# Kernel tuning notes

Hardware: AMD Instinct MI355X
Metric: run time of the kernel (lower is better)

## Reference

```python
import jax, jax.numpy as jnp
import numpy as np
import math

N_LEVELS = 16
F_PER_LEVEL = 2
LOG2_T = 19
T = 1 << LOG2_T
BASE_RES = 16
MAX_RES = 2048
PER_LEVEL_SCALE = (MAX_RES / BASE_RES) ** (1.0 / (N_LEVELS - 1))
BOUND = 0.5
PRIMES = (np.uint32(1), np.uint32(2654435761), np.uint32(805459861))


def _weight_norm(v, g):
    # w = g * v / ||v||_row (torch weight_norm over dim=1)
    return v * (g / jnp.linalg.norm(v, axis=1))[:, None]


def _softplus100(x):
    # torch Softplus(beta=100)
    return jax.nn.softplus(100.0 * x) * 0.01


def hashgrid_encode(x01, table):
    # x01: [N,3] in [0,1]; table: [L, T, F]
    feats = []
    for l in range(N_LEVELS):
        scale = BASE_RES * (PER_LEVEL_SCALE ** l) - 1.0  # tcnn grid scale
        res = int(math.ceil(scale)) + 1
        pos = x01 * scale + 0.5
        pos_floor = jnp.floor(pos)
        w = pos - pos_floor                      # [N,3] trilinear fracs
        c0 = pos_floor.astype(jnp.uint32)        # [N,3] base corner
        dense = (res ** 3) <= T                  # static per level
        acc = jnp.zeros((x01.shape[0], F_PER_LEVEL), dtype=table.dtype)
        for corner in range(8):
            off = [(corner >> d) & 1 for d in range(3)]
            cx = c0[:, 0] + np.uint32(off[0])
            cy = c0[:, 1] + np.uint32(off[1])
            cz = c0[:, 2] + np.uint32(off[2])
            if dense:
                idx = cx + cy * np.uint32(res) + cz * np.uint32(res * res)
            else:
                idx = (cx * PRIMES[0]) ^ (cy * PRIMES[1]) ^ (cz * PRIMES[2])
                idx = idx & np.uint32(T - 1)
            wc = ((w[:, 0] if off[0] else 1.0 - w[:, 0])
                  * (w[:, 1] if off[1] else 1.0 - w[:, 1])
                  * (w[:, 2] if off[2] else 1.0 - w[:, 2]))
            acc = acc + wc[:, None] * table[l, idx.astype(jnp.int32)]
        feats.append(acc)
    return jnp.concatenate(feats, axis=-1)  # [N, 32]


def setup_inputs() -> dict:
    key = jax.random.key(0)
    ks = jax.random.split(key, 4)
    N = 2 ** 21
    x = jax.random.uniform(ks[0], (N, 3), jnp.float32, -BOUND, BOUND)
    table = jax.random.uniform(ks[1], (N_LEVELS, T, F_PER_LEVEL), jnp.float32, -1e-4, 1e-4)
    d_in, d_hid, d_out = 35, 64, 13
    v1 = jax.random.normal(ks[2], (d_hid, d_in), jnp.float32) * (math.sqrt(2) / math.sqrt(d_hid))
    v2 = jax.random.normal(ks[3], (d_out, d_hid), jnp.float32) * 1e-4 + math.sqrt(math.pi) / math.sqrt(d_hid)
    g1 = jnp.linalg.norm(v1, axis=1)
    g2 = jnp.linalg.norm(v2, axis=1)
    b1 = jnp.zeros((d_hid,), jnp.float32)
    b2 = jnp.full((d_out,), -0.5, jnp.float32)  # -sphere_init_radius
    return {"x": x, "table": table, "v1": v1, "g1": g1, "b1": b1,
            "v2": v2, "g2": g2, "b2": b2}


def reference(x, table, v1, g1, b1, v2, g2, b2):
    x01 = jnp.clip((x + BOUND) / (2.0 * BOUND), 0.0, 1.0)
    enc = hashgrid_encode(x01, table)            # [N, 32]
    h = jnp.concatenate([x, enc], axis=1)        # [N, 35]
    w1 = _weight_norm(v1, g1)
    w2 = _weight_norm(v2, g2)
    h = _softplus100(h @ w1.T + b1)
    out = h @ w2.T + b2                          # [N, 13]
    return out
```

## Files before the change

### kernel.cpp

```cpp
#include <hip/hip_runtime.h>
#include <hip/hip_fp16.h>
#include <cstdint>
#include <cmath>

#define NLEV 16
#define NHASH 11
#define NHENC 9
#define NDENSE 5
#define TBL (1u << 19)
#define NBKT 32768
#define PTS 2

typedef _Float16 half8 __attribute__((ext_vector_type(8)));
typedef float f32x4 __attribute__((ext_vector_type(4)));

struct LevelParams {
    float scale[NLEV];
    uint32_t res[NLEV];
    uint32_t hashed_mask;
};

__device__ __forceinline__ int krow_map(int kr) {
    if (kr <= 2) return kr;
    if (kr >= 4 && kr <= 13) return kr - 1;
    if (kr >= 16 && kr <= 37) return kr - 3;
    return -1;
}

__global__ __launch_bounds__(256) void prep_weights(
    const float* __restrict__ v1, const float* __restrict__ g1,
    const float* __restrict__ v2, const float* __restrict__ g2,
    float* __restrict__ w1t, float* __restrict__ w2n,
    __half* __restrict__ w1f, __half* __restrict__ w2f)
{
    int t = threadIdx.x;
    if (t < 64) {
        float s = 0.f;
        #pragma unroll
        for (int k = 0; k < 35; ++k) { float v = v1[t*35 + k]; s += v*v; }
        float f = g1[t] / sqrtf(s);
        #pragma unroll
        for (int k = 0; k < 35; ++k) w1t[k*64 + t] = v1[t*35 + k] * f;
    } else if (t < 77) {
        int r = t - 64;
        float s = 0.f;
        #pragma unroll
        for (int k = 0; k < 64; ++k) { float v = v2[r*64 + k]; s += v*v; }
        float f = g2[r] / sqrtf(s);
        #pragma unroll
        for (int k = 0; k < 64; ++k) w2n[r*64 + k] = v2[r*64 + k] * f;
    }
    __syncthreads();
    for (int i = t; i < 4096; i += 256) {
        int j = i & 7, lane = (i >> 3) & 63, nt = (i >> 9) & 3, kc = i >> 11;
        int kr = kc*32 + ((lane >> 4) << 3) + j;
        int ncol = nt*16 + (lane & 15);
        int m = krow_map(kr);
        float val = (m >= 0) ? w1t[m*64 + ncol] : 0.f;
        w1f[i] = __float2half(val);
    }
    for (int i = t; i < 1024; i += 256) {
        int j = i & 7, lane = (i >> 3) & 63, kc = i >> 9;
        int kr = kc*32 + ((lane >> 4) << 3) + j;
        int col = lane & 15;
        float val = (col < 13) ? w2n[col*64 + kr] : 0.f;
        w2f[i] = __float2half(val);
    }
}

__device__ __forceinline__ uint32_t bucket_key(float u0, float u1, float u2)
{
    uint32_t a = min(31u, (uint32_t)(u0 * 32.f));
    uint32_t b = min(31u, (uint32_t)(u1 * 32.f));
    uint32_t c = min(31u, (uint32_t)(u2 * 32.f));
    return (a << 10) | (b << 5) | c;
}

__device__ __forceinline__ void load_u(const float* __restrict__ x, int pp,
                                       float& u0, float& u1, float& u2)
{
    float x0 = x[3*(size_t)pp + 0];
    float x1 = x[3*(size_t)pp + 1];
    float x2 = x[3*(size_t)pp + 2];
    u0 = fminf(fmaxf(x0 + 0.5f, 0.f), 1.f);
    u1 = fminf(fmaxf(x1 + 0.5f, 0.f), 1.f);
    u2 = fminf(fmaxf(x2 + 0.5f, 0.f), 1.f);
}

__global__ __launch_bounds__(256) void pack_and_hist(
    const float2* __restrict__ tin, uint32_t* __restrict__ tout, int n_entries,
    const float* __restrict__ x, uint32_t* __restrict__ hist, int N,
    int packBlocks)
{
    int b = blockIdx.x;
    if (b < packBlocks) {
        int i = b * 256 + threadIdx.x;
        if (i < n_entries) {
            float2 v = tin[i];
            __half2 h = __floats2half2_rn(v.x, v.y);
            tout[i] = *reinterpret_cast<uint32_t*>(&h);
        }
    } else {
        int i = (b - packBlocks) * 256 + threadIdx.x;
        if (i < N) {
            float u0, u1, u2;
            load_u(x, i, u0, u1, u2);
            atomicAdd(&hist[bucket_key(u0, u1, u2)], 1u);
        }
    }
}

__global__ __launch_bounds__(1024) void scan_hist(
    const uint32_t* __restrict__ hist, uint32_t* __restrict__ offs)
{
    __shared__ uint32_t part[1024];
    int t = threadIdx.x;
    uint32_t loc[32];
    uint32_t s = 0;
    #pragma unroll
    for (int k = 0; k < 32; ++k) { loc[k] = s; s += hist[t*32 + k]; }
    part[t] = s;
    __syncthreads();
    for (int d = 1; d < 1024; d <<= 1) {
        uint32_t v = (t >= d) ? part[t - d] : 0u;
        __syncthreads();
        part[t] += v;
        __syncthreads();
    }
    uint32_t base = (t > 0) ? part[t - 1] : 0u;
    #pragma unroll
    for (int k = 0; k < 32; ++k) offs[t*32 + k] = base + loc[k];
}

__global__ __launch_bounds__(256) void scatter_kernel(
    const float* __restrict__ x, uint32_t* __restrict__ offs,
    float4* __restrict__ xs4, int N)
{
    int i = blockIdx.x * 256 + threadIdx.x;
    if (i < N) {
        float x0 = x[3*(size_t)i + 0];
        float x1 = x[3*(size_t)i + 1];
        float x2 = x[3*(size_t)i + 2];
        float u0 = fminf(fmaxf(x0 + 0.5f, 0.f), 1.f);
        float u1 = fminf(fmaxf(x1 + 0.5f, 0.f), 1.f);
        float u2 = fminf(fmaxf(x2 + 0.5f, 0.f), 1.f);
        uint32_t pos = atomicAdd(&offs[bucket_key(u0, u1, u2)], 1u);
        xs4[pos] = make_float4(x0, x1, x2, __int_as_float(i));
    }
}

__device__ __forceinline__ void encode_one(
    float u0, float u1, float u2, float s, uint32_t res, bool hashed,
    const uint32_t* __restrict__ tl, float& a0, float& a1)
{
    float px = u0 * s + 0.5f;
    float py = u1 * s + 0.5f;
    float pz = u2 * s + 0.5f;
    float fx = floorf(px), fy = floorf(py), fz = floorf(pz);
    float wx1 = px - fx, wy1 = py - fy, wz1 = pz - fz;
    float wx0 = 1.f - wx1, wy0 = 1.f - wy1, wz0 = 1.f - wz1;
    uint32_t cx = (uint32_t)fx, cy = (uint32_t)fy, cz = (uint32_t)fz;

    uint32_t ix0, ix1, iy0, iy1, iz0, iz1;
    if (hashed) {
        ix0 = cx;                 ix1 = cx + 1u;
        iy0 = cy * 2654435761u;   iy1 = (cy + 1u) * 2654435761u;
        iz0 = cz * 805459861u;    iz1 = (cz + 1u) * 805459861u;
    } else {
        ix0 = cx;                 ix1 = cx + 1u;
        iy0 = cy * res;           iy1 = iy0 + res;
        uint32_t rr = res * res;
        iz0 = cz * rr;            iz1 = iz0 + rr;
    }

    uint32_t idxs[8];
    #pragma unroll
    for (int c = 0; c < 8; ++c) {
        uint32_t jx = (c & 1) ? ix1 : ix0;
        uint32_t jy = (c & 2) ? iy1 : iy0;
        uint32_t jz = (c & 4) ? iz1 : iz0;
        idxs[c] = hashed ? ((jx ^ jy ^ jz) & (TBL - 1u)) : (jx + jy + jz);
    }
    uint32_t raw[8];
    #pragma unroll
    for (int c = 0; c < 8; ++c) raw[c] = tl[idxs[c]];

    float wxy00 = wx0*wy0, wxy10 = wx1*wy0, wxy01 = wx0*wy1, wxy11 = wx1*wy1;
    a0 = 0.f; a1 = 0.f;
    #pragma unroll
    for (int c = 0; c < 8; ++c) {
        float wxy = (c & 2) ? ((c & 1) ? wxy11 : wxy01)
                            : ((c & 1) ? wxy10 : wxy00);
        float w = wxy * ((c & 4) ? wz1 : wz0);
        __half2 hv = *reinterpret_cast<__half2*>(&raw[c]);
        float2 v = __half22float2(hv);
        a0 += w * v.x;
        a1 += w * v.y;
    }
}

template <int SORTED>
__global__ __launch_bounds__(256) void encode_hashed(
    const float* __restrict__ x, const float4* __restrict__ xs4,
    const uint32_t* __restrict__ tpk,
    uint32_t* __restrict__ feats, int N, int chunks_per_level, LevelParams P)
{
    int bid = blockIdx.x;
    int li = bid / chunks_per_level;
    int l = li + 7;
    int base = (bid - li * chunks_per_level) * (256*PTS) + threadIdx.x;
    const uint32_t* tl = tpk + (size_t)l * TBL;
    float s = P.scale[l];

    int p[PTS];
    #pragma unroll
    for (int t = 0; t < PTS; ++t) p[t] = base + t * 256;

    uint2 Q[PTS][4];
    uint32_t par[PTS];
    float wx0[PTS], wx1[PTS], wyz[PTS][4];

    #pragma unroll
    for (int t = 0; t < PTS; ++t) {
        int pp = (p[t] < N) ? p[t] : (N - 1);
        float u0, u1, u2;
        if (SORTED) {
            float4 v4 = xs4[pp];
            u0 = fminf(fmaxf(v4.x + 0.5f, 0.f), 1.f);
            u1 = fminf(fmaxf(v4.y + 0.5f, 0.f), 1.f);
            u2 = fminf(fmaxf(v4.z + 0.5f, 0.f), 1.f);
        } else {
            load_u(x, pp, u0, u1, u2);
        }

        float px = u0 * s + 0.5f;
        float py = u1 * s + 0.5f;
        float pz = u2 * s + 0.5f;
        float fx = floorf(px), fy = floorf(py), fz = floorf(pz);
        float a1f = px - fx, b1f = py - fy, c1f = pz - fz;
        wx1[t] = a1f; wx0[t] = 1.f - a1f;
        float wy0 = 1.f - b1f, wz0 = 1.f - c1f;
        uint32_t cx = (uint32_t)fx, cy = (uint32_t)fy, cz = (uint32_t)fz;

        wyz[t][0] = wy0 * wz0;
        wyz[t][1] = b1f * wz0;
        wyz[t][2] = wy0 * c1f;
        wyz[t][3] = b1f * c1f;

        uint32_t hy0 = cy * 2654435761u, hy1 = (cy + 1u) * 2654435761u;
        uint32_t hz0 = cz * 805459861u,  hz1 = (cz + 1u) * 805459861u;
        uint32_t r[4] = { hy0 ^ hz0, hy1 ^ hz0, hy0 ^ hz1, hy1 ^ hz1 };

        par[t] = 0u;
        if (!(cx & 1u)) {
            #pragma unroll
            for (int k = 0; k < 4; ++k) {
                uint32_t v0 = (cx ^ r[k]) & (TBL - 1u);
                Q[t][k] = *reinterpret_cast<const uint2*>(tl + (v0 & ~1u));
                par[t] |= (v0 & 1u) << k;
            }
        } else {
            #pragma unroll
            for (int k = 0; k < 4; ++k) {
                uint32_t v0 = (cx ^ r[k]) & (TBL - 1u);
                uint32_t v1 = ((cx + 1u) ^ r[k]) & (TBL - 1u);
                Q[t][k].x = tl[v0];
                Q[t][k].y = tl[v1];
            }
        }
    }

    #pragma unroll
    for (int t = 0; t < PTS; ++t) {
        float a0 = 0.f, a1 = 0.f;
        #pragma unroll
        for (int k = 0; k < 4; ++k) {
            uint32_t swap = (par[t] >> k) & 1u;
            uint32_t b0 = swap ? Q[t][k].y : Q[t][k].x;
            uint32_t b1 = swap ? Q[t][k].x : Q[t][k].y;
            __half2 h0 = *reinterpret_cast<__half2*>(&b0);
            __half2 h1 = *reinterpret_cast<__half2*>(&b1);
            float2 c0 = __half22float2(h0);
            float2 c1 = __half22float2(h1);
            a0 += wyz[t][k] * (wx0[t] * c0.x + wx1[t] * c1.x);
            a1 += wyz[t][k] * (wx0[t] * c0.y + wx1[t] * c1.y);
        }
        __half2 hv = __floats2half2_rn(a0, a1);
        if (p[t] < N) {
            __builtin_nontemporal_store(*reinterpret_cast<uint32_t*>(&hv),
                                        &feats[(size_t)li * N + p[t]]);
        }
    }
}

__global__ __launch_bounds__(256) void mlp_mfma(
    const float4* __restrict__ xs4,
    const uint32_t* __restrict__ tpk,
    const uint32_t* __restrict__ feats,
    const __half* __restrict__ w1f,
    const __half* __restrict__ w2f,
    const float* __restrict__ b1,
    const float* __restrict__ b2,
    float* __restrict__ out, int N, LevelParams P)
{
    __shared__ uint4 ldsA[4][576];
    __shared__ int   ldsI[4][64];
    int wid = threadIdx.x >> 6, lane = threadIdx.x & 63;
    int wpt = blockIdx.x * 256 + wid * 64;
    int pt = wpt + lane;
    int pp = (pt < N) ? pt : (N - 1);

    float4 v4 = xs4[pp];
    float x0 = v4.x, x1 = v4.y, x2 = v4.z;
    ldsI[wid][lane] = __float_as_int(v4.w);
    float u0 = fminf(fmaxf(x0 + 0.5f, 0.f), 1.f);
    float u1 = fminf(fmaxf(x1 + 0.5f, 0.f), 1.f);
    float u2 = fminf(fmaxf(x2 + 0.5f, 0.f), 1.f);

    uint32_t dw[32];
    #pragma unroll
    for (int i = 0; i < 32; ++i) dw[i] = 0u;
    __half2 h01 = __floats2half2_rn(x0, x1);
    __half2 h2_ = __floats2half2_rn(x2, 0.f);
    dw[0] = *reinterpret_cast<uint32_t*>(&h01);
    dw[1] = *reinterpret_cast<uint32_t*>(&h2_);
    #pragma unroll
    for (int l = 0; l < NDENSE; ++l) {
        const uint32_t* tl = tpk + (size_t)l * TBL;
        float a0, a1;
        encode_one(u0, u1, u2, P.scale[l], P.res[l], false, tl, a0, a1);
        __half2 hv = __floats2half2_rn(a0, a1);
        dw[2 + l] = *reinterpret_cast<uint32_t*>(&hv);
    }
    #pragma unroll
    for (int l = 5; l <= 6; ++l) {
        const uint32_t* tl = tpk + (size_t)l * TBL;
        float a0, a1;
        encode_one(u0, u1, u2, P.scale[l], P.res[l], true, tl, a0, a1);
        __half2 hv = __floats2half2_rn(a0, a1);
        dw[8 + (l - 5)] = *reinterpret_cast<uint32_t*>(&hv);
    }
    #pragma unroll
    for (int li = 0; li < NHENC; ++li)
        dw[10 + li] = feats[(size_t)li * N + pp];

    #pragma unroll
    for (int c = 0; c < 8; ++c) {
        uint4 ch = make_uint4(dw[4*c], dw[4*c+1], dw[4*c+2], dw[4*c+3]);
        ldsA[wid][c*64 + lane] = ch;
    }

    const uint4* w1f4 = (const uint4*)w1f;
    half8 bf[4][2];
    #pragma unroll
    for (int nt = 0; nt < 4; ++nt)
        #pragma unroll
        for (int kc = 0; kc < 2; ++kc) {
            uint4 u = w1f4[(kc*4 + nt)*64 + lane];
            bf[nt][kc] = __builtin_bit_cast(half8, u);
        }

    f32x4 C[4][4];
    #pragma unroll
    for (int nt = 0; nt < 4; ++nt) {
        float bv = b1[nt*16 + (lane & 15)];
        #pragma unroll
        for (int m = 0; m < 4; ++m) C[m][nt] = f32x4{bv, bv, bv, bv};
    }

    #pragma unroll
    for (int m = 0; m < 4; ++m) {
        uint4 ua0 = ldsA[wid][((lane >> 4)      )*64 + m*16 + (lane & 15)];
        uint4 ua1 = ldsA[wid][((lane >> 4) + 4  )*64 + m*16 + (lane & 15)];
        half8 a0 = __builtin_bit_cast(half8, ua0);
        half8 a1 = __builtin_bit_cast(half8, ua1);
        #pragma unroll
        for (int nt = 0; nt < 4; ++nt) {
            C[m][nt] = __builtin_amdgcn_mfma_f32_16x16x32_f16(a0, bf[nt][0], C[m][nt], 0, 0, 0);
            C[m][nt] = __builtin_amdgcn_mfma_f32_16x16x32_f16(a1, bf[nt][1], C[m][nt], 0, 0, 0);
        }
    }

    #pragma unroll
    for (int m = 0; m < 4; ++m)
        #pragma unroll
        for (int nt = 0; nt < 4; ++nt)
            #pragma unroll
            for (int r = 0; r < 4; ++r) {
                float z = 100.f * C[m][nt][r];
                float t = __expf(-fabsf(z));
                C[m][nt][r] = (fmaxf(z, 0.f) + __logf(1.f + t)) * 0.01f;
            }

    uint32_t* hl = (uint32_t*)&ldsA[wid][0];
    bool evenl = (lane & 1) == 0;
    #pragma unroll
    for (int m = 0; m < 4; ++m)
        #pragma unroll
        for (int nt = 0; nt < 4; ++nt)
            #pragma unroll
            for (int r = 0; r < 4; ++r) {
                float self = C[m][nt][r];
                float other = __shfl_xor(self, 1);
                if (evenl) {
                    __half2 hp = __floats2half2_rn(self, other);
                    int prow = m*16 + ((lane >> 4) << 2) + r;
                    int colp = (nt*16 + (lane & 15)) >> 1;
                    hl[prow*36 + colp] = *reinterpret_cast<uint32_t*>(&hp);
                }
            }

    const uint4* w2f4 = (const uint4*)w2f;
    half8 b2f[2];
    #pragma unroll
    for (int kc = 0; kc < 2; ++kc) {
        uint4 u = w2f4[kc*64 + lane];
        b2f[kc] = __builtin_bit_cast(half8, u);
    }
    int col = lane & 15;
    float b2v = (col < 13) ? b2[col] : 0.f;

    #pragma unroll
    for (int m = 0; m < 4; ++m) {
        uint4 ua0 = ldsA[wid][(m*16 + col)*9 + 0 + (lane >> 4)];
        uint4 ua1 = ldsA[wid][(m*16 + col)*9 + 4 + (lane >> 4)];
        f32x4 c2 = f32x4{b2v, b2v, b2v, b2v};
        c2 = __builtin_amdgcn_mfma_f32_16x16x32_f16(
                 __builtin_bit_cast(half8, ua0), b2f[0], c2, 0, 0, 0);
        c2 = __builtin_amdgcn_mfma_f32_16x16x32_f16(
                 __builtin_bit_cast(half8, ua1), b2f[1], c2, 0, 0, 0);
        #pragma unroll
        for (int r = 0; r < 4; ++r) {
            int prow = m*16 + ((lane >> 4) << 2) + r;
            if (col < 13 && wpt + prow < N) {
                int og = ldsI[wid][prow];
                out[(size_t)og * 13 + col] = c2[r];
            }
        }
    }
}

__global__ __launch_bounds__(256) void mlp_dense_scalar(
    const float* __restrict__ x, const uint32_t* __restrict__ tpk,
    const uint32_t* __restrict__ feats,
    const float* __restrict__ w1t, const float* __restrict__ b1,
    const float* __restrict__ w2, const float* __restrict__ b2,
    float* __restrict__ out, int N, LevelParams P)
{
    int p = blockIdx.x * 256 + threadIdx.x;
    bool valid = (p < N);
    int pp = valid ? p : (N - 1);

    float u0, u1, u2;
    load_u(x, pp, u0, u1, u2);
    float x0 = x[3*(size_t)pp + 0];
    float x1 = x[3*(size_t)pp + 1];
    float x2 = x[3*(size_t)pp + 2];

    uint32_t rf[NHENC];
    #pragma unroll
    for (int li = 0; li < NHENC; ++li) rf[li] = feats[(size_t)li * N + pp];

    float h[64];
    #pragma unroll
    for (int j = 0; j < 64; ++j)
        h[j] = b1[j] + x0 * w1t[0*64 + j] + x1 * w1t[1*64 + j] + x2 * w1t[2*64 + j];

    #pragma unroll
    for (int l = 0; l < 7; ++l) {
        const uint32_t* tl = tpk + (size_t)l * TBL;
        float a0, a1;
        encode_one(u0, u1, u2, P.scale[l], P.res[l], l >= NDENSE, tl, a0, a1);
        const float* c0p = w1t + (3 + 2*l) * 64;
        const float* c1p = c0p + 64;
        #pragma unroll
        for (int j = 0; j < 64; ++j) h[j] += a0 * c0p[j] + a1 * c1p[j];
    }
    #pragma unroll
    for (int li = 0; li < NHENC; ++li) {
        __half2 hv = *reinterpret_cast<__half2*>(&rf[li]);
        float2 f = __half22float2(hv);
        int l = li + 7;
        const float* c0p = w1t + (3 + 2*l) * 64;
        const float* c1p = c0p + 64;
        #pragma unroll
        for (int j = 0; j < 64; ++j) h[j] += f.x * c0p[j] + f.y * c1p[j];
    }
    #pragma unroll
    for (int j = 0; j < 64; ++j) {
        float z = 100.f * h[j];
        float t = __expf(-fabsf(z));
        h[j] = (fmaxf(z, 0.f) + __logf(1.f + t)) * 0.01f;
    }
    float* op = out + (size_t)pp * 13;
    for (int o = 0; o < 13; ++o) {
        float a = b2[o];
        const float* wr = w2 + o * 64;
        #pragma unroll
        for (int k = 0; k < 64; ++k) a = fmaf(h[k], wr[k], a);
        if (valid) op[o] = a;
    }
}

template <int PACKED>
__global__ __launch_bounds__(256) void sdf_fused(
    const float* __restrict__ x, const void* __restrict__ table,
    const float* __restrict__ w1t, const float* __restrict__ b1,
    const float* __restrict__ w2, const float* __restrict__ b2,
    float* __restrict__ out, int N, LevelParams P)
{
    int i = blockIdx.x * 256 + threadIdx.x;
    bool valid = (i < N);
    int ii = valid ? i : (N - 1);

    float x0 = x[3*(size_t)ii + 0];
    float x1 = x[3*(size_t)ii + 1];
    float x2 = x[3*(size_t)ii + 2];
    float u0 = fminf(fmaxf(x0 + 0.5f, 0.f), 1.f);
    float u1 = fminf(fmaxf(x1 + 0.5f, 0.f), 1.f);
    float u2 = fminf(fmaxf(x2 + 0.5f, 0.f), 1.f);

    float h[64];
    #pragma unroll
    for (int j = 0; j < 64; ++j)
        h[j] = b1[j] + x0 * w1t[0*64 + j] + x1 * w1t[1*64 + j] + x2 * w1t[2*64 + j];

    for (int l = 0; l < NLEV; ++l) {
        bool hashed = (P.hashed_mask >> l) & 1u;
        float a0, a1;
        if (PACKED) {
            const uint32_t* tl = (const uint32_t*)table + (size_t)l * TBL;
            encode_one(u0, u1, u2, P.scale[l], P.res[l], hashed, tl, a0, a1);
        } else {
            const float* tl = (const float*)table + (size_t)l * (size_t)(TBL * 2u);
            float s = P.scale[l]; uint32_t res = P.res[l];
            float px = u0*s + 0.5f, py = u1*s + 0.5f, pz = u2*s + 0.5f;
            float fx = floorf(px), fy = floorf(py), fz = floorf(pz);
            float wx1 = px-fx, wy1 = py-fy, wz1 = pz-fz;
            float wx0 = 1.f-wx1, wy0 = 1.f-wy1, wz0 = 1.f-wz1;
            uint32_t cx = (uint32_t)fx, cy = (uint32_t)fy, cz = (uint32_t)fz;
            a0 = 0.f; a1 = 0.f;
            #pragma unroll
            for (int c = 0; c < 8; ++c) {
                uint32_t jx = cx + (c & 1);
                uint32_t jy = cy + ((c >> 1) & 1);
                uint32_t jz = cz + ((c >> 2) & 1);
                uint32_t idx = hashed
                    ? ((jx ^ (jy * 2654435761u) ^ (jz * 805459861u)) & (TBL - 1u))
                    : (jx + jy * res + jz * res * res);
                float w = ((c & 1) ? wx1 : wx0) * ((c & 2) ? wy1 : wy0)
                        * ((c & 4) ? wz1 : wz0);
                float2 v = *reinterpret_cast<const float2*>(tl + (size_t)idx * 2u);
                a0 += w * v.x; a1 += w * v.y;
            }
        }
        const float* c0p = w1t + (3 + 2*l) * 64;
        const float* c1p = c0p + 64;
        #pragma unroll
        for (int j = 0; j < 64; ++j) h[j] += a0 * c0p[j] + a1 * c1p[j];
    }

    #pragma unroll
    for (int j = 0; j < 64; ++j) {
        float z = 100.f * h[j];
        float t = __expf(-fabsf(z));
        h[j] = (fmaxf(z, 0.f) + __logf(1.f + t)) * 0.01f;
    }

    float* op = out + (size_t)ii * 13;
    for (int o = 0; o < 13; ++o) {
        float a = b2[o];
        const float* wr = w2 + o * 64;
        #pragma unroll
        for (int k = 0; k < 64; ++k) a += h[k] * wr[k];
        if (valid) op[o] = a;
    }
}

extern "C" void kernel_launch(void* const* d_in, const int* in_sizes, int n_in,
                              void* d_out, int out_size, void* d_ws, size_t ws_size,
                              hipStream_t stream)
{
    const float* x     = (const float*)d_in[0];
    const float* table = (const float*)d_in[1];
    const float* v1    = (const float*)d_in[2];
    const float* g1    = (const float*)d_in[3];
    const float* b1    = (const float*)d_in[4];
    const float* v2    = (const float*)d_in[5];
    const float* g2    = (const float*)d_in[6];
    const float* b2    = (const float*)d_in[7];
    float* out = (float*)d_out;
    int N = in_sizes[0] / 3;

    const int n_entries = NLEV * (int)TBL;
    const size_t packed_bytes = (size_t)n_entries * 4u;
    const size_t xs4_bytes    = (size_t)N * 16u;
    const size_t feats_bytes  = (size_t)NHENC * (size_t)N * 4u;
    const size_t hist_bytes   = (size_t)NBKT * 4u;
    const size_t w_bytes      = (35*64 + 13*64) * sizeof(float);
    const size_t wf_bytes     = (4096 + 1024) * sizeof(__half);

    size_t off_packed = 0;
    size_t off_xs4    = off_packed + packed_bytes;
    size_t off_feats  = off_xs4 + xs4_bytes;
    size_t off_w      = off_feats + feats_bytes;
    size_t off_wf     = off_w + w_bytes;
    size_t sorted_need = off_wf + wf_bytes;
    bool overlay_ok = feats_bytes >= 2 * hist_bytes;

    bool sorted_ok = (ws_size >= sorted_need) && overlay_ok;
    bool two_pass  = (ws_size >= packed_bytes + feats_bytes + w_bytes + wf_bytes);
    bool packed_ok = (ws_size >= packed_bytes + w_bytes + wf_bytes);

    uint32_t* tpk   = (uint32_t*)((char*)d_ws + off_packed);
    float4*   xs4   = (float4*)((char*)d_ws + off_xs4);
    uint32_t* feats;
    float* w1t;
    if (sorted_ok) {
        feats = (uint32_t*)((char*)d_ws + off_feats);
        w1t = (float*)((char*)d_ws + off_w);
    } else if (two_pass) {
        feats = (uint32_t*)((char*)d_ws + packed_bytes);
        w1t = (float*)((char*)d_ws + packed_bytes + feats_bytes);
    } else {
        feats = nullptr;
        w1t = (float*)((char*)d_ws + (packed_ok ? packed_bytes : 0));
    }
    uint32_t* hist = feats;
    uint32_t* offs = feats + NBKT;
    float* w2n = w1t + 35 * 64;
    __half* w1f = (__half*)(w2n + 13 * 64);
    __half* w2f = w1f + 4096;

    LevelParams P;
    P.hashed_mask = 0u;
    double pls = pow(128.0, 1.0 / 15.0);
    for (int l = 0; l < NLEV; ++l) {
        double sc = 16.0 * pow(pls, (double)l) - 1.0;
        P.scale[l] = (float)sc;
        uint32_t res = (uint32_t)(ceil(sc)) + 1u;
        P.res[l] = res;
        uint64_t r3 = (uint64_t)res * res * res;
        if (r3 > (uint64_t)TBL) P.hashed_mask |= (1u << l);
    }

    prep_weights<<<1, 256, 0, stream>>>(v1, g1, v2, g2, w1t, w2n, w1f, w2f);

    int chunks = (N + 255) / 256;
    int packBlocks = (n_entries + 255) / 256;
    if (sorted_ok) {
        hipMemsetAsync(hist, 0, hist_bytes, stream);
        pack_and_hist<<<packBlocks + chunks, 256, 0, stream>>>(
            (const float2*)table, tpk, n_entries, x, hist, N, packBlocks);
        scan_hist<<<1, 1024, 0, stream>>>(hist, offs);
        scatter_kernel<<<chunks, 256, 0, stream>>>(x, offs, xs4, N);
        int chunksE = (N + 256*PTS - 1) / (256*PTS);
        encode_hashed<1><<<chunksE * NHENC, 256, 0, stream>>>(
            x, xs4, tpk, feats, N, chunksE, P);
        mlp_mfma<<<chunks, 256, 0, stream>>>(
            xs4, tpk, feats, w1f, w2f, b1, b2, out, N, P);
    } else if (two_pass) {
        pack_and_hist<<<packBlocks, 256, 0, stream>>>(
            (const float2*)table, tpk, n_entries, x, nullptr, 0, packBlocks);
        int chunksE = (N + 256*PTS - 1) / (256*PTS);
        encode_hashed<0><<<chunksE * NHENC, 256, 0, stream>>>(
            x, nullptr, tpk, feats, N, chunksE, P);
        mlp_dense_scalar<<<chunks, 256, 0, stream>>>(
            x, tpk, feats, w1t, b1, w2n, b2, out, N, P);
    } else if (packed_ok) {
        pack_and_hist<<<packBlocks, 256, 0, stream>>>(
            (const float2*)table, tpk, n_entries, x, nullptr, 0, packBlocks);
        sdf_fused<1><<<chunks, 256, 0, stream>>>(
            x, (const void*)tpk, w1t, b1, w2n, b2, out, N, P);
    } else {
        sdf_fused<0><<<chunks, 256, 0, stream>>>(
            x, (const void*)table, w1t, b1, w2n, b2, out, N, P);
    }
}
```

Baseline: 709.9 us.

## Quantize hash table to int8 with global absmax scale

Replaces the fp16-packed hash table with an int8 packing of two features per entry. The per-tensor scale comes from a new max-abs reduction kernel over the fp32 table. This halves table footprint and gather bytes, and the paired-corner loads now cover four entries per 8-byte load. In exchange it adds a full extra pass over the table for the reduction and loses precision, since values are quantized to 8 bits with a single global scale.

```diff
diff --git a/kernel.cpp b/kernel.cpp
--- a/kernel.cpp
+++ b/kernel.cpp
@@ -4,7 +4,6 @@
 #include <cmath>
 
 #define NLEV 16
-#define NHASH 11
 #define NHENC 9
 #define NDENSE 5
 #define TBL (1u << 19)
@@ -68,6 +67,17 @@
     }
 }
 
+__global__ __launch_bounds__(256) void max_reduce(
+    const float* __restrict__ t, uint32_t* __restrict__ scaleU, int n)
+{
+    int i = blockIdx.x * 256 + threadIdx.x;
+    float m = 0.f;
+    for (int k = i; k < n; k += gridDim.x * 256) m = fmaxf(m, fabsf(t[k]));
+    #pragma unroll
+    for (int o = 32; o >= 1; o >>= 1) m = fmaxf(m, __shfl_xor(m, o));
+    if ((threadIdx.x & 63) == 0) atomicMax(scaleU, __float_as_uint(m));
+}
+
 __device__ __forceinline__ uint32_t bucket_key(float u0, float u1, float u2)
 {
     uint32_t a = min(31u, (uint32_t)(u0 * 32.f));
@@ -87,20 +97,31 @@
     u2 = fminf(fmaxf(x2 + 0.5f, 0.f), 1.f);
 }
 
+__device__ __forceinline__ uint32_t quant8(float v, float qs)
+{
+    int q = (int)rintf(v * qs);
+    q = max(-127, min(127, q));
+    return (uint32_t)(q & 0xff);
+}
+
 __global__ __launch_bounds__(256) void pack_and_hist(
-    const float2* __restrict__ tin, uint32_t* __restrict__ tout, int n_entries,
+    const float2* __restrict__ tin, uint32_t* __restrict__ tout, int n_half,
     const float* __restrict__ x, uint32_t* __restrict__ hist, int N,
-    int packBlocks)
+    int packBlocks, const uint32_t* __restrict__ scaleU)
 {
     int b = blockIdx.x;
     if (b < packBlocks) {
         int i = b * 256 + threadIdx.x;
-        if (i < n_entries) {
-            float2 v = tin[i];
-            __half2 h = __floats2half2_rn(v.x, v.y);
-            tout[i] = *reinterpret_cast<uint32_t*>(&h);
-        }
-    } else {
+        if (i < n_half) {
+            float smax = fmaxf(__uint_as_float(*scaleU), 1e-30f);
+            float qs = 127.f / smax;
+            float2 a = tin[2*(size_t)i];
+            float2 c = tin[2*(size_t)i + 1];
+            uint32_t w = quant8(a.x, qs) | (quant8(a.y, qs) << 8)
+                       | (quant8(c.x, qs) << 16) | (quant8(c.y, qs) << 24);
+            tout[i] = w;
+        }
+    } else if (hist) {
         int i = (b - packBlocks) * 256 + threadIdx.x;
         if (i < N) {
             float u0, u1, u2;
@@ -149,9 +170,9 @@
     }
 }
 
-__device__ __forceinline__ void encode_one(
+__device__ __forceinline__ void encode_one8(
     float u0, float u1, float u2, float s, uint32_t res, bool hashed,
-    const uint32_t* __restrict__ tl, float& a0, float& a1)
+    const uint16_t* __restrict__ t16, float deq, float& a0, float& a1)
 {
     float px = u0 * s + 0.5f;
     float py = u1 * s + 0.5f;
@@ -181,9 +202,9 @@
         uint32_t jz = (c & 4) ? iz1 : iz0;
         idxs[c] = hashed ? ((jx ^ jy ^ jz) & (TBL - 1u)) : (jx + jy + jz);
     }
-    uint32_t raw[8];
-    #pragma unroll
-    for (int c = 0; c < 8; ++c) raw[c] = tl[idxs[c]];
+    uint16_t raw[8];
+    #pragma unroll
+    for (int c = 0; c < 8; ++c) raw[c] = t16[idxs[c]];
 
     float wxy00 = wx0*wy0, wxy10 = wx1*wy0, wxy01 = wx0*wy1, wxy11 = wx1*wy1;
     a0 = 0.f; a1 = 0.f;
@@ -192,25 +213,29 @@
         float wxy = (c & 2) ? ((c & 1) ? wxy11 : wxy01)
                             : ((c & 1) ? wxy10 : wxy00);
         float w = wxy * ((c & 4) ? wz1 : wz0);
-        __half2 hv = *reinterpret_cast<__half2*>(&raw[c]);
-        float2 v = __half22float2(hv);
-        a0 += w * v.x;
-        a1 += w * v.y;
-    }
+        float f0 = (float)(int8_t)(raw[c] & 0xff);
+        float f1 = (float)(int8_t)(raw[c] >> 8);
+        a0 += w * f0;
+        a1 += w * f1;
+    }
+    a0 *= deq;
+    a1 *= deq;
 }
 
 template <int SORTED>
 __global__ __launch_bounds__(256) void encode_hashed(
     const float* __restrict__ x, const float4* __restrict__ xs4,
-    const uint32_t* __restrict__ tpk,
-    uint32_t* __restrict__ feats, int N, int chunks_per_level, LevelParams P)
+    const uint8_t* __restrict__ tpk8,
+    uint32_t* __restrict__ feats, int N, int chunks_per_level,
+    const uint32_t* __restrict__ scaleU, LevelParams P)
 {
     int bid = blockIdx.x;
     int li = bid / chunks_per_level;
     int l = li + 7;
     int base = (bid - li * chunks_per_level) * (256*PTS) + threadIdx.x;
-    const uint32_t* tl = tpk + (size_t)l * TBL;
+    const uint8_t* tb8 = tpk8 + (size_t)l * TBL * 2u;
     float s = P.scale[l];
+    float deq = __uint_as_float(*scaleU) * (1.f / 127.f);
 
     int p[PTS];
     #pragma unroll
@@ -251,23 +276,26 @@
         uint32_t hz0 = cz * 805459861u,  hz1 = (cz + 1u) * 805459861u;
         uint32_t r[4] = { hy0 ^ hz0, hy1 ^ hz0, hy0 ^ hz1, hy1 ^ hz1 };
 
-        par[t] = 0u;
-        if (!(cx & 1u)) {
+        uint32_t pr = 0u;
+        if ((cx & 3u) != 3u) {
             #pragma unroll
             for (int k = 0; k < 4; ++k) {
                 uint32_t v0 = (cx ^ r[k]) & (TBL - 1u);
-                Q[t][k] = *reinterpret_cast<const uint2*>(tl + (v0 & ~1u));
-                par[t] |= (v0 & 1u) << k;
+                uint32_t v1 = ((cx + 1u) ^ r[k]) & (TBL - 1u);
+                Q[t][k] = *reinterpret_cast<const uint2*>(tb8 + ((v0 & ~3u) << 1));
+                pr |= ((v0 & 3u) | ((v1 & 3u) << 2)) << (4*k);
             }
         } else {
             #pragma unroll
             for (int k = 0; k < 4; ++k) {
                 uint32_t v0 = (cx ^ r[k]) & (TBL - 1u);
                 uint32_t v1 = ((cx + 1u) ^ r[k]) & (TBL - 1u);
-                Q[t][k].x = tl[v0];
-                Q[t][k].y = tl[v1];
+                Q[t][k].x = *reinterpret_cast<const uint32_t*>(tb8 + ((v0 & ~1u) << 1));
+                Q[t][k].y = *reinterpret_cast<const uint32_t*>(tb8 + ((v1 & ~1u) << 1));
+                pr |= ((v0 & 1u) | (((v1 & 1u) | 2u) << 2)) << (4*k);
             }
         }
+        par[t] = pr;
     }
 
     #pragma unroll
@@ -275,17 +303,20 @@
         float a0 = 0.f, a1 = 0.f;
         #pragma unroll
         for (int k = 0; k < 4; ++k) {
-            uint32_t swap = (par[t] >> k) & 1u;
-            uint32_t b0 = swap ? Q[t][k].y : Q[t][k].x;
-            uint32_t b1 = swap ? Q[t][k].x : Q[t][k].y;
-            __half2 h0 = *reinterpret_cast<__half2*>(&b0);
-            __half2 h1 = *reinterpret_cast<__half2*>(&b1);
-            float2 c0 = __half22float2(h0);
-            float2 c1 = __half22float2(h1);
-            a0 += wyz[t][k] * (wx0[t] * c0.x + wx1[t] * c1.x);
-            a1 += wyz[t][k] * (wx0[t] * c0.y + wx1[t] * c1.y);
-        }
-        __half2 hv = __floats2half2_rn(a0, a1);
+            uint32_t pk = par[t] >> (4*k);
+            uint32_t j0 = pk & 3u, j1 = (pk >> 2) & 3u;
+            uint32_t w0 = (j0 & 2u) ? Q[t][k].y : Q[t][k].x;
+            uint32_t w1 = (j1 & 2u) ? Q[t][k].y : Q[t][k].x;
+            uint32_t e0 = (j0 & 1u) ? (w0 >> 16) : (w0 & 0xffffu);
+            uint32_t e1 = (j1 & 1u) ? (w1 >> 16) : (w1 & 0xffffu);
+            float c0x = (float)(int8_t)(e0 & 0xff);
+            float c0y = (float)(int8_t)(e0 >> 8);
+            float c1x = (float)(int8_t)(e1 & 0xff);
+            float c1y = (float)(int8_t)(e1 >> 8);
+            a0 += wyz[t][k] * (wx0[t] * c0x + wx1[t] * c1x);
+            a1 += wyz[t][k] * (wx0[t] * c0y + wx1[t] * c1y);
+        }
+        __half2 hv = __floats2half2_rn(a0 * deq, a1 * deq);
         if (p[t] < N) {
             __builtin_nontemporal_store(*reinterpret_cast<uint32_t*>(&hv),
                                         &feats[(size_t)li * N + p[t]]);
@@ -295,12 +326,13 @@
 
 __global__ __launch_bounds__(256) void mlp_mfma(
     const float4* __restrict__ xs4,
-    const uint32_t* __restrict__ tpk,
+    const uint8_t* __restrict__ tpk8,
     const uint32_t* __restrict__ feats,
     const __half* __restrict__ w1f,
     const __half* __restrict__ w2f,
     const float* __restrict__ b1,
     const float* __restrict__ b2,
+    const uint32_t* __restrict__ scaleU,
     float* __restrict__ out, int N, LevelParams P)
 {
     __shared__ uint4 ldsA[4][576];
@@ -316,6 +348,7 @@
     float u0 = fminf(fmaxf(x0 + 0.5f, 0.f), 1.f);
     float u1 = fminf(fmaxf(x1 + 0.5f, 0.f), 1.f);
     float u2 = fminf(fmaxf(x2 + 0.5f, 0.f), 1.f);
+    float deq = __uint_as_float(*scaleU) * (1.f / 127.f);
 
     uint32_t dw[32];
     #pragma unroll
@@ -326,17 +359,17 @@
     dw[1] = *reinterpret_cast<uint32_t*>(&h2_);
     #pragma unroll
     for (int l = 0; l < NDENSE; ++l) {
-        const uint32_t* tl = tpk + (size_t)l * TBL;
+        const uint16_t* t16 = (const uint16_t*)(tpk8 + (size_t)l * TBL * 2u);
         float a0, a1;
-        encode_one(u0, u1, u2, P.scale[l], P.res[l], false, tl, a0, a1);
+        encode_one8(u0, u1, u2, P.scale[l], P.res[l], false, t16, deq, a0, a1);
         __half2 hv = __floats2half2_rn(a0, a1);
         dw[2 + l] = *reinterpret_cast<uint32_t*>(&hv);
     }
     #pragma unroll
     for (int l = 5; l <= 6; ++l) {
-        const uint32_t* tl = tpk + (size_t)l * TBL;
+        const uint16_t* t16 = (const uint16_t*)(tpk8 + (size_t)l * TBL * 2u);
         float a0, a1;
-        encode_one(u0, u1, u2, P.scale[l], P.res[l], true, tl, a0, a1);
+        encode_one8(u0, u1, u2, P.scale[l], P.res[l], true, t16, deq, a0, a1);
         __half2 hv = __floats2half2_rn(a0, a1);
         dw[8 + (l - 5)] = *reinterpret_cast<uint32_t*>(&hv);
     }
@@ -441,10 +474,11 @@
 }
 
 __global__ __launch_bounds__(256) void mlp_dense_scalar(
-    const float* __restrict__ x, const uint32_t* __restrict__ tpk,
+    const float* __restrict__ x, const uint8_t* __restrict__ tpk8,
     const uint32_t* __restrict__ feats,
     const float* __restrict__ w1t, const float* __restrict__ b1,
     const float* __restrict__ w2, const float* __restrict__ b2,
+    const uint32_t* __restrict__ scaleU,
     float* __restrict__ out, int N, LevelParams P)
 {
     int p = blockIdx.x * 256 + threadIdx.x;
@@ -456,6 +490,7 @@
     float x0 = x[3*(size_t)pp + 0];
     float x1 = x[3*(size_t)pp + 1];
     float x2 = x[3*(size_t)pp + 2];
+    float deq = __uint_as_float(*scaleU) * (1.f / 127.f);
 
     uint32_t rf[NHENC];
     #pragma unroll
@@ -468,9 +503,9 @@
 
     #pragma unroll
     for (int l = 0; l < 7; ++l) {
-        const uint32_t* tl = tpk + (size_t)l * TBL;
+        const uint16_t* t16 = (const uint16_t*)(tpk8 + (size_t)l * TBL * 2u);
         float a0, a1;
-        encode_one(u0, u1, u2, P.scale[l], P.res[l], l >= NDENSE, tl, a0, a1);
+        encode_one8(u0, u1, u2, P.scale[l], P.res[l], l >= NDENSE, t16, deq, a0, a1);
         const float* c0p = w1t + (3 + 2*l) * 64;
         const float* c1p = c0p + 64;
         #pragma unroll
@@ -502,9 +537,8 @@
     }
 }
 
-template <int PACKED>
-__global__ __launch_bounds__(256) void sdf_fused(
-    const float* __restrict__ x, const void* __restrict__ table,
+__global__ __launch_bounds__(256) void sdf_fused_f32(
+    const float* __restrict__ x, const float* __restrict__ table,
     const float* __restrict__ w1t, const float* __restrict__ b1,
     const float* __restrict__ w2, const float* __restrict__ b2,
     float* __restrict__ out, int N, LevelParams P)
@@ -527,32 +561,26 @@
 
     for (int l = 0; l < NLEV; ++l) {
         bool hashed = (P.hashed_mask >> l) & 1u;
-        float a0, a1;
-        if (PACKED) {
-            const uint32_t* tl = (const uint32_t*)table + (size_t)l * TBL;
-            encode_one(u0, u1, u2, P.scale[l], P.res[l], hashed, tl, a0, a1);
-        } else {
-            const float* tl = (const float*)table + (size_t)l * (size_t)(TBL * 2u);
-            float s = P.scale[l]; uint32_t res = P.res[l];
-            float px = u0*s + 0.5f, py = u1*s + 0.5f, pz = u2*s + 0.5f;
-            float fx = floorf(px), fy = floorf(py), fz = floorf(pz);
-            float wx1 = px-fx, wy1 = py-fy, wz1 = pz-fz;
-            float wx0 = 1.f-wx1, wy0 = 1.f-wy1, wz0 = 1.f-wz1;
-            uint32_t cx = (uint32_t)fx, cy = (uint32_t)fy, cz = (uint32_t)fz;
-            a0 = 0.f; a1 = 0.f;
-            #pragma unroll
-            for (int c = 0; c < 8; ++c) {
-                uint32_t jx = cx + (c & 1);
-                uint32_t jy = cy + ((c >> 1) & 1);
-                uint32_t jz = cz + ((c >> 2) & 1);
-                uint32_t idx = hashed
-                    ? ((jx ^ (jy * 2654435761u) ^ (jz * 805459861u)) & (TBL - 1u))
-                    : (jx + jy * res + jz * res * res);
-                float w = ((c & 1) ? wx1 : wx0) * ((c & 2) ? wy1 : wy0)
-                        * ((c & 4) ? wz1 : wz0);
-                float2 v = *reinterpret_cast<const float2*>(tl + (size_t)idx * 2u);
-                a0 += w * v.x; a1 += w * v.y;
-            }
+        const float* tl = table + (size_t)l * (size_t)(TBL * 2u);
+        float s = P.scale[l]; uint32_t res = P.res[l];
+        float px = u0*s + 0.5f, py = u1*s + 0.5f, pz = u2*s + 0.5f;
+        float fx = floorf(px), fy = floorf(py), fz = floorf(pz);
+        float wx1 = px-fx, wy1 = py-fy, wz1 = pz-fz;
+        float wx0 = 1.f-wx1, wy0 = 1.f-wy1, wz0 = 1.f-wz1;
+        uint32_t cx = (uint32_t)fx, cy = (uint32_t)fy, cz = (uint32_t)fz;
+        float a0 = 0.f, a1 = 0.f;
+        #pragma unroll
+        for (int c = 0; c < 8; ++c) {
+            uint32_t jx = cx + (c & 1);
+            uint32_t jy = cy + ((c >> 1) & 1);
+            uint32_t jz = cz + ((c >> 2) & 1);
+            uint32_t idx = hashed
+                ? ((jx ^ (jy * 2654435761u) ^ (jz * 805459861u)) & (TBL - 1u))
+                : (jx + jy * res + jz * res * res);
+            float w = ((c & 1) ? wx1 : wx0) * ((c & 2) ? wy1 : wy0)
+                    * ((c & 4) ? wz1 : wz0);
+            float2 v = *reinterpret_cast<const float2*>(tl + (size_t)idx * 2u);
+            a0 += w * v.x; a1 += w * v.y;
         }
         const float* c0p = w1t + (3 + 2*l) * 64;
         const float* c1p = c0p + 64;
@@ -593,44 +621,46 @@
     int N = in_sizes[0] / 3;
 
     const int n_entries = NLEV * (int)TBL;
-    const size_t packed_bytes = (size_t)n_entries * 4u;
-    const size_t xs4_bytes    = (size_t)N * 16u;
-    const size_t feats_bytes  = (size_t)NHENC * (size_t)N * 4u;
-    const size_t hist_bytes   = (size_t)NBKT * 4u;
-    const size_t w_bytes      = (35*64 + 13*64) * sizeof(float);
-    const size_t wf_bytes     = (4096 + 1024) * sizeof(__half);
-
-    size_t off_packed = 0;
-    size_t off_xs4    = off_packed + packed_bytes;
-    size_t off_feats  = off_xs4 + xs4_bytes;
-    size_t off_w      = off_feats + feats_bytes;
-    size_t off_wf     = off_w + w_bytes;
-    size_t sorted_need = off_wf + wf_bytes;
+    const size_t tpk8_bytes  = (size_t)n_entries * 2u;
+    const size_t xs4_bytes   = (size_t)N * 16u;
+    const size_t feats_bytes = (size_t)NHENC * (size_t)N * 4u;
+    const size_t hist_bytes  = (size_t)NBKT * 4u;
+    const size_t w_bytes     = (35*64 + 13*64) * sizeof(float);
+    const size_t wf_bytes    = (4096 + 1024) * sizeof(__half);
+
+    size_t off_tpk8  = 0;
+    size_t off_xs4   = off_tpk8 + tpk8_bytes;
+    size_t off_feats = off_xs4 + xs4_bytes;
+    size_t off_w     = off_feats + feats_bytes;
+    size_t off_wf    = off_w + w_bytes;
+    size_t off_scale = off_wf + wf_bytes;
+    size_t sorted_need = off_scale + 16;
     bool overlay_ok = feats_bytes >= 2 * hist_bytes;
 
     bool sorted_ok = (ws_size >= sorted_need) && overlay_ok;
-    bool two_pass  = (ws_size >= packed_bytes + feats_bytes + w_bytes + wf_bytes);
-    bool packed_ok = (ws_size >= packed_bytes + w_bytes + wf_bytes);
-
-    uint32_t* tpk   = (uint32_t*)((char*)d_ws + off_packed);
-    float4*   xs4   = (float4*)((char*)d_ws + off_xs4);
+    bool two_pass  = (ws_size >= tpk8_bytes + feats_bytes + w_bytes + wf_bytes + 16);
+    bool packed_ok = (ws_size >= tpk8_bytes + w_bytes + wf_bytes + 16);
+
+    uint8_t* tpk8 = (uint8_t*)((char*)d_ws + off_tpk8);
+    float4*  xs4  = (float4*)((char*)d_ws + off_xs4);
     uint32_t* feats;
     float* w1t;
     if (sorted_ok) {
         feats = (uint32_t*)((char*)d_ws + off_feats);
         w1t = (float*)((char*)d_ws + off_w);
     } else if (two_pass) {
-        feats = (uint32_t*)((char*)d_ws + packed_bytes);
-        w1t = (float*)((char*)d_ws + packed_bytes + feats_bytes);
+        feats = (uint32_t*)((char*)d_ws + tpk8_bytes);
+        w1t = (float*)((char*)d_ws + tpk8_bytes + feats_bytes);
     } else {
         feats = nullptr;
-        w1t = (float*)((char*)d_ws + (packed_ok ? packed_bytes : 0));
+        w1t = (float*)((char*)d_ws + (packed_ok ? tpk8_bytes : 0));
     }
     uint32_t* hist = feats;
-    uint32_t* offs = feats + NBKT;
+    uint32_t* offs = feats ? feats + NBKT : nullptr;
     float* w2n = w1t + 35 * 64;
     __half* w1f = (__half*)(w2n + 13 * 64);
     __half* w2f = w1f + 4096;
+    uint32_t* scaleU = (uint32_t*)(w2f + 1024);
 
     LevelParams P;
     P.hashed_mask = 0u;
@@ -647,33 +677,35 @@
     prep_weights<<<1, 256, 0, stream>>>(v1, g1, v2, g2, w1t, w2n, w1f, w2f);
 
     int chunks = (N + 255) / 256;
-    int packBlocks = (n_entries + 255) / 256;
+    int n_half = n_entries / 2;
+    int packBlocks = (n_half + 255) / 256;
     if (sorted_ok) {
         hipMemsetAsync(hist, 0, hist_bytes, stream);
+        hipMemsetAsync(scaleU, 0, 4, stream);
+        max_reduce<<<2048, 256, 0, stream>>>(table, scaleU, n_entries * 2);
         pack_and_hist<<<packBlocks + chunks, 256, 0, stream>>>(
-            (const float2*)table, tpk, n_entries, x, hist, N, packBlocks);
+            (const float2*)table, (uint32_t*)tpk8, n_half, x, hist, N,
+            packBlocks, scaleU);
         scan_hist<<<1, 1024, 0, stream>>>(hist, offs);
         scatter_kernel<<<chunks, 256, 0, stream>>>(x, offs, xs4, N);
         int chunksE = (N + 256*PTS - 1) / (256*PTS);
         encode_hashed<1><<<chunksE * NHENC, 256, 0, stream>>>(
-            x, xs4, tpk, feats, N, chunksE, P);
+            x, xs4, tpk8, feats, N, chunksE, scaleU, P);
         mlp_mfma<<<chunks, 256, 0, stream>>>(
-            xs4, tpk, feats, w1f, w2f, b1, b2, out, N, P);
+            xs4, tpk8, feats, w1f, w2f, b1, b2, scaleU, out, N, P);
     } else if (two_pass) {
+        hipMemsetAsync(scaleU, 0, 4, stream);
+        max_reduce<<<2048, 256, 0, stream>>>(table, scaleU, n_entries * 2);
         pack_and_hist<<<packBlocks, 256, 0, stream>>>(
-            (const float2*)table, tpk, n_entries, x, nullptr, 0, packBlocks);
+            (const float2*)table, (uint32_t*)tpk8, n_half, x, nullptr, 0,
+            packBlocks, scaleU);
         int chunksE = (N + 256*PTS - 1) / (256*PTS);
         encode_hashed<0><<<chunksE * NHENC, 256, 0, stream>>>(
-            x, nullptr, tpk, feats, N, chunksE, P);
+            x, nullptr, tpk8, feats, N, chunksE, scaleU, P);
         mlp_dense_scalar<<<chunks, 256, 0, stream>>>(
-            x, tpk, feats, w1t, b1, w2n, b2, out, N, P);
-    } else if (packed_ok) {
-        pack_and_hist<<<packBlocks, 256, 0, stream>>>(
-            (const float2*)table, tpk, n_entries, x, nullptr, 0, packBlocks);
-        sdf_fused<1><<<chunks, 256, 0, stream>>>(
-            x, (const void*)tpk, w1t, b1, w2n, b2, out, N, P);
+            x, tpk8, feats, w1t, b1, w2n, b2, scaleU, out, N, P);
     } else {
-        sdf_fused<0><<<chunks, 256, 0, stream>>>(
-            x, (const void*)table, w1t, b1, w2n, b2, out, N, P);
-    }
-}
+        sdf_fused_f32<<<chunks, 256, 0, stream>>>(
+            x, table, w1t, b1, w2n, b2, out, N, P);
+    }
+}
```

Result: slower. 813.1 us (+14.5%).
